# Performance work log

Hardware: AMD Instinct MI355X
Metric: run time of the kernel (lower is better)

The kernel has to match this reference:

```python
import jax, jax.numpy as jnp
import numpy as np

B, S, D, H = 4, 2048, 1024, 16
DH = D // H
NEG = -100000.0


def setup_inputs() -> dict:
    key = jax.random.key(0)
    ks = jax.random.split(key, 13)
    s = 1.0 / np.sqrt(D)
    inp = {
        'q': jax.random.normal(ks[0], (B, S, D), jnp.float32),
        'k': jax.random.normal(ks[1], (B, S, D), jnp.float32),
        'v': jax.random.normal(ks[2], (B, S, D), jnp.float32),
        'mask': jax.random.randint(ks[3], (B, 1, S, S), 0, 2).astype(bool),
        'wq_w': jax.random.normal(ks[4], (D, D), jnp.float32) * s,
        'wq_b': jnp.zeros((D,), jnp.float32),
        'wk_w': jax.random.normal(ks[5], (D, D), jnp.float32) * s,
        'wk_b': jnp.zeros((D,), jnp.float32),
        'wv_w': jax.random.normal(ks[6], (D, D), jnp.float32) * s,
        'wv_b': jnp.zeros((D,), jnp.float32),
        'wo_w': jax.random.normal(ks[7], (D, D), jnp.float32) * s,
        'wo_b': jnp.zeros((D,), jnp.float32),
    }
    return inp


def reference(q, k, v, mask, wq_w, wq_b, wk_w, wk_b, wv_w, wv_b, wo_w, wo_b):
    # torch Linear: y = x @ W^T + b
    qh = (q @ wq_w.T + wq_b).reshape(B, S, H, DH).transpose(0, 2, 1, 3)  # [B,H,S,DH]
    kh = (k @ wk_w.T + wk_b).reshape(B, S, H, DH).transpose(0, 2, 1, 3)
    vh = (v @ wv_w.T + wv_b).reshape(B, S, H, DH).transpose(0, 2, 1, 3)
    # NOTE: original code has NO 1/sqrt(d) scaling
    alpha = jnp.einsum('bhqd,bhkd->bhqk', qh, kh)  # [B,H,S,S]
    alpha = jnp.where(mask, NEG, alpha)
    score = jax.nn.softmax(alpha, axis=-1)
    x = jnp.einsum('bhqk,bhkd->bhqd', score, vh)
    x = x.transpose(0, 2, 1, 3).reshape(B, S, D)
    return x @ wo_w.T + wo_b
```

## Files before the change

### kernel.cpp

```cpp
#include <hip/hip_runtime.h>
#include <hip/hip_bf16.h>

#define B_ 4
#define S_ 2048
#define D_ 1024
#define H_ 16
#define NEGV (-100000.0f)
#define L2E 1.4426950408889634f

typedef __attribute__((ext_vector_type(8))) short short8;
typedef __attribute__((ext_vector_type(4))) float f32x4;
typedef unsigned short us;
typedef unsigned long long u64;

__device__ __forceinline__ us f2h(float f) {
  union { _Float16 h; us u; } c;
  c.h = (_Float16)f;
  return c.u;
}
__device__ __forceinline__ float exp2a(float x) {
  float r;
  asm("v_exp_f32 %0, %1" : "=v"(r) : "v"(x));
  return r;
}

__global__ void detect_mask_kernel(const int* __restrict__ mi, int* __restrict__ flag) {
  int t = threadIdx.x;
  bool bad = false;
  for (int i = t; i < 16384; i += 64) {
    int v = mi[i];
    bad = bad || (v != 0 && v != 1);
  }
  unsigned long long any = __ballot(bad);
  if (t == 0) flag[0] = (any != 0ull) ? 1 : 0;
}

__global__ __launch_bounds__(256) void pack_mask(const void* __restrict__ maskp,
                                                 const int* __restrict__ flag,
                                                 unsigned* __restrict__ pk) {
  int w = blockIdx.x * 256 + threadIdx.x;
  unsigned bits = 0;
  if (flag[0]) {
    const uint4* p = (const uint4*)((const unsigned char*)maskp + (size_t)w * 32);
#pragma unroll
    for (int q = 0; q < 2; ++q) {
      uint4 v = p[q];
      unsigned vv[4] = {v.x, v.y, v.z, v.w};
#pragma unroll
      for (int e = 0; e < 4; ++e) {
        unsigned byte4 = vv[e];
#pragma unroll
        for (int bb = 0; bb < 4; ++bb)
          bits |= (unsigned)(((byte4 >> (8 * bb)) & 0xffu) != 0) << (q * 16 + e * 4 + bb);
      }
    }
  } else {
    const uint4* p = (const uint4*)((const int*)maskp + (size_t)w * 32);
#pragma unroll
    for (int q = 0; q < 8; ++q) {
      uint4 v = p[q];
      bits |= (unsigned)(v.x != 0) << (q * 4 + 0);
      bits |= (unsigned)(v.y != 0) << (q * 4 + 1);
      bits |= (unsigned)(v.z != 0) << (q * 4 + 2);
      bits |= (unsigned)(v.w != 0) << (q * 4 + 3);
    }
  }
  pk[w] = bits;
}

__global__ __launch_bounds__(256) void cvt_f16x3(const float* __restrict__ i0,
                                                 const float* __restrict__ i1,
                                                 const float* __restrict__ i2,
                                                 us* __restrict__ o0, us* __restrict__ o1,
                                                 us* __restrict__ o2) {
  int z = blockIdx.x >> 12;
  int i = (blockIdx.x & 4095) * 256 + threadIdx.x;
  const float* in = z == 0 ? i0 : z == 1 ? i1 : i2;
  us* out = z == 0 ? o0 : z == 1 ? o1 : o2;
  float4 a = ((const float4*)in)[2 * i];
  float4 b = ((const float4*)in)[2 * i + 1];
  us u[8] = {f2h(a.x), f2h(a.y), f2h(a.z), f2h(a.w),
             f2h(b.x), f2h(b.y), f2h(b.z), f2h(b.w)};
  ((uint4*)out)[i] = *(uint4*)u;
}

__global__ __launch_bounds__(256) void cvt_w4(const float* __restrict__ w0,
                                              const float* __restrict__ w1,
                                              const float* __restrict__ w2,
                                              const float* __restrict__ w3,
                                              us* __restrict__ d0, us* __restrict__ d1,
                                              us* __restrict__ d2, us* __restrict__ d3) {
  int which = blockIdx.x >> 9;
  int i = (blockIdx.x & 511) * 256 + threadIdx.x;
  const float* w = which == 0 ? w0 : which == 1 ? w1 : which == 2 ? w2 : w3;
  us* d = which == 0 ? d0 : which == 1 ? d1 : which == 2 ? d2 : d3;
  float4 a = ((const float4*)w)[2 * i];
  float4 b = ((const float4*)w)[2 * i + 1];
  us u[8] = {f2h(a.x), f2h(a.y), f2h(a.z), f2h(a.w),
             f2h(b.x), f2h(b.y), f2h(b.z), f2h(b.w)};
  ((uint4*)d)[i] = *(uint4*)u;
}

__device__ __forceinline__ void gload16(const us* g, us* l) {
  __builtin_amdgcn_global_load_lds((const __attribute__((address_space(1))) void*)g,
                                   (__attribute__((address_space(3))) void*)l, 16, 0, 0);
}

__device__ __forceinline__ int swzb(int row, int c16) {
  return row * 128 + ((c16 ^ (row & 7)) << 4);
}

template <int OMODE>
__global__ __launch_bounds__(256) void gemm_mfma(
    const us* __restrict__ A0, const us* __restrict__ A1, const us* __restrict__ A2,
    const us* __restrict__ Wp0, const us* __restrict__ Wp1, const us* __restrict__ Wp2,
    const float* __restrict__ b0, const float* __restrict__ b1, const float* __restrict__ b2,
    void* __restrict__ C0, void* __restrict__ C1, void* __restrict__ C2,
    int M, int N, int K) {
  __shared__ __align__(16) us As[2][128 * 64];
  __shared__ __align__(16) us Ws[2][128 * 64];

  const int z = blockIdx.z;
  const us* A = z == 0 ? A0 : z == 1 ? A1 : A2;
  const us* W = z == 0 ? Wp0 : z == 1 ? Wp1 : Wp2;
  const float* bias = z == 0 ? b0 : z == 1 ? b1 : b2;
  void* Cp = z == 0 ? C0 : z == 1 ? C1 : C2;

  const int m0 = blockIdx.x * 128;
  const int n0 = blockIdx.y * 128;
  const int t = threadIdx.x;
  const int w = t >> 6, l = t & 63;
  const int l15 = l & 15, l4 = l >> 4;
  const int wm = w >> 1, wn = w & 1;

  int goff[4];
#pragma unroll
  for (int j = 0; j < 4; ++j) {
    int u = t + j * 256;
    int r = u >> 3, c8 = u & 7;
    int g = c8 ^ (r & 7);
    goff[j] = r * K + g * 8;
  }
  const us* Ag = A + (size_t)m0 * K;
  const us* Wg = W + (size_t)n0 * K;

  f32x4 acc[4][4];
#pragma unroll
  for (int m = 0; m < 4; ++m)
#pragma unroll
    for (int n = 0; n < 4; ++n) acc[m][n] = (f32x4){0.f, 0.f, 0.f, 0.f};

  auto stage = [&](int k0, int bb) {
#pragma unroll
    for (int j = 0; j < 4; ++j) {
      int u = t + j * 256;
      gload16(Ag + goff[j] + k0, &As[bb][u * 8]);
      gload16(Wg + goff[j] + k0, &Ws[bb][u * 8]);
    }
  };

  stage(0, 0);
  __syncthreads();
  int cur = 0;
  for (int k0 = 0; k0 < K; k0 += 64) {
    if (k0 + 64 < K) stage(k0 + 64, cur ^ 1);
#pragma unroll
    for (int ks = 0; ks < 2; ++ks) {
      short8 ah[4], bh_[4];
#pragma unroll
      for (int m = 0; m < 4; ++m)
        ah[m] = *(const short8*)((const char*)As[cur] + swzb(wm * 64 + m * 16 + l15, ks * 4 + l4));
#pragma unroll
      for (int n = 0; n < 4; ++n)
        bh_[n] = *(const short8*)((const char*)Ws[cur] + swzb(wn * 64 + n * 16 + l15, ks * 4 + l4));
#pragma unroll
      for (int m = 0; m < 4; ++m)
#pragma unroll
        for (int n = 0; n < 4; ++n)
          acc[m][n] = __builtin_amdgcn_mfma_f32_16x16x32_f16(ah[m], bh_[n], acc[m][n], 0, 0, 0);
    }
    __syncthreads();
    cur ^= 1;
  }

  float bv[4];
#pragma unroll
  for (int n = 0; n < 4; ++n) bv[n] = bias[n0 + wn * 64 + n * 16 + l15];

#pragma unroll
  for (int m = 0; m < 4; ++m) {
#pragma unroll
    for (int i = 0; i < 4; ++i) {
      int gm = m0 + wm * 64 + m * 16 + l4 * 4 + i;
#pragma unroll
      for (int n = 0; n < 4; ++n) {
        int gn = n0 + wn * 64 + n * 16 + l15;
        float o = acc[m][n][i] + bv[n];
        if constexpr (OMODE == 0) {
          ((float*)Cp)[(size_t)gm * N + gn] = o;
        } else {
          int b = gm >> 11, s = gm & (S_ - 1);
          int hh = gn >> 6, d = gn & 63;
          size_t idx = (((size_t)(b * H_ + hh) << 11) + s) * 64 + d;
          ((us*)Cp)[idx] = f2h(o);
        }
      }
    }
  }
}

__global__ __launch_bounds__(256) void transpose_v(const us* __restrict__ vh,
                                                   us* __restrict__ vt) {
  __shared__ us Ts[64][72];
  int blk = blockIdx.x;
  int bh = blk >> 5, s0 = (blk & 31) << 6;
  int t = threadIdx.x;
#pragma unroll
  for (int p = 0; p < 2; ++p) {
    int c = t + p * 256;
    int rs = c >> 3, c8 = c & 7;
    *(uint4*)&Ts[rs][c8 * 8] = *(const uint4*)(vh + ((size_t)bh * S_ + s0 + rs) * 64 + c8 * 8);
  }
  __syncthreads();
#pragma unroll
  for (int p = 0; p < 2; ++p) {
    int c = t + p * 256;
    int rd = c >> 3, s8 = c & 7;
    union { us u[8]; uint4 v; } tmp;
#pragma unroll
    for (int e = 0; e < 8; ++e) tmp.u[e] = Ts[s8 * 8 + e][rd];
    *(uint4*)(vt + ((size_t)bh * 64 + rd) * S_ + s0 + s8 * 8) = tmp.v;
  }
}

__device__ __forceinline__ int swz(int row, int bc) {
  return (row << 7) + (bc ^ ((row & 7) << 4));
}

__global__ __launch_bounds__(512) void attn_mfma(
    const us* __restrict__ qh, const us* __restrict__ kh,
    const us* __restrict__ vt, const unsigned* __restrict__ pk,
    us* __restrict__ xout) {
  __shared__ __align__(16) us Ks[2][4096];
  __shared__ __align__(16) us Vs[2][4096];
  __shared__ __align__(16) char Ps[16384];

  const int blk = ((blockIdx.x & 7) << 7) + (blockIdx.x >> 3);
  const int bh = blk >> 4;
  const int q0 = (blk & 15) << 7;
  const int b = bh >> 4, h = bh & (H_ - 1);
  const int t = threadIdx.x;
  const int w = t >> 6, l = t & 63;
  const int l15 = l & 15, l4 = l >> 4;

  short8 qf[2];
  {
    const size_t qbase = ((size_t)bh * S_ + q0 + 16 * w + l15) * 64 + l4 * 8;
    qf[0] = *(const short8*)(qh + qbase);
    qf[1] = *(const short8*)(qh + qbase + 32);
  }

  f32x4 accO[4];
#pragma unroll
  for (int jd = 0; jd < 4; ++jd) accO[jd] = (f32x4){0.f, 0.f, 0.f, 0.f};
  float m_i = -1e30f, l_p = 0.f;

  const int r_st = t >> 3, c_st = (t & 7) ^ ((t >> 3) & 7);
  const us* kh_src = kh + ((size_t)bh * S_ + r_st) * 64 + c_st * 8;
  const us* vt_src = vt + ((size_t)bh * 64 + r_st) * S_ + c_st * 8;

  auto stage = [&](int k0, int bb) {
    gload16(kh_src + (size_t)k0 * 64, &Ks[bb][t * 8]);
    gload16(vt_src + k0, &Vs[bb][t * 8]);
  };

  stage(0, 0);
  __syncthreads();
  int cur = 0;

  char* Pw = Ps + w * 2048;
  const int prowb = l15 * 128;
  const int rr7 = l15 & 7;
  const int bhalf = l4 >> 1;
  const int wsub = (l4 & 1) * 8;
  const unsigned* pb = pk + ((size_t)b * S_ + q0 + 16 * w + l15) * (S_ / 32);

  for (int k0 = 0; k0 < S_; k0 += 64) {
    uint2 mw = *(const uint2*)(pb + (k0 >> 5));
    if (k0 + 64 < S_) stage(k0 + 64, cur ^ 1);

    const char* KT = (const char*)Ks[cur];
    const char* VT = (const char*)Vs[cur];

    __builtin_amdgcn_s_setprio(1);
    f32x4 sj[4];
#pragma unroll
    for (int j = 0; j < 4; ++j) {
      f32x4 s = {0.f, 0.f, 0.f, 0.f};
#pragma unroll
      for (int c = 0; c < 2; ++c) {
        short8 kf = *(const short8*)(KT + swz(l15 + 16 * j, l4 * 16 + 64 * c));
        s = __builtin_amdgcn_mfma_f32_16x16x32_f16(kf, qf[c], s, 0, 0, 0);
      }
      sj[j] = s;
    }
    __builtin_amdgcn_s_setprio(0);

    float tm = -3e38f;
#pragma unroll
    for (int j = 0; j < 4; ++j) {
      unsigned wrd = (j < 2) ? mw.x : mw.y;
      int bb = ((j & 1) << 4) + (l4 << 2);
#pragma unroll
      for (int i = 0; i < 4; ++i) {
        float bf = (float)((wrd >> (bb + i)) & 1u);
        sj[j][i] = fmaf(bf, NEGV, sj[j][i]);
      }
      tm = fmaxf(tm, fmaxf(fmaxf(sj[j][0], sj[j][1]), fmaxf(sj[j][2], sj[j][3])));
    }
    tm = fmaxf(tm, __shfl_xor(tm, 16));
    tm = fmaxf(tm, __shfl_xor(tm, 32));

    if (__any(tm - m_i > 8.0f)) {
      float mnew = fmaxf(m_i, tm);
      float scl = exp2a((m_i - mnew) * L2E);
      l_p *= scl;
      m_i = mnew;
      float sr0 = __shfl(scl, 4 * l4 + 0);
      float sr1 = __shfl(scl, 4 * l4 + 1);
      float sr2 = __shfl(scl, 4 * l4 + 2);
      float sr3 = __shfl(scl, 4 * l4 + 3);
#pragma unroll
      for (int jd = 0; jd < 4; ++jd) {
        accO[jd][0] *= sr0; accO[jd][1] *= sr1;
        accO[jd][2] *= sr2; accO[jd][3] *= sr3;
      }
    }

    float ml2 = m_i * L2E;
#pragma unroll
    for (int j = 0; j < 4; ++j) {
      float p0 = exp2a(fmaf(sj[j][0], L2E, -ml2));
      float p1 = exp2a(fmaf(sj[j][1], L2E, -ml2));
      float p2 = exp2a(fmaf(sj[j][2], L2E, -ml2));
      float p3 = exp2a(fmaf(sj[j][3], L2E, -ml2));
      l_p += (p0 + p1) + (p2 + p3);
      unsigned d0, d1;
      asm("v_cvt_pkrtz_f16_f32 %0, %1, %2" : "=v"(d0) : "v"(p0), "v"(p1));
      asm("v_cvt_pkrtz_f16_f32 %0, %1, %2" : "=v"(d1) : "v"(p2), "v"(p3));
      int chunk = ((j << 1) | bhalf) ^ rr7;
      *(u64*)(Pw + prowb + (chunk << 4) + wsub) = (u64)d0 | ((u64)d1 << 32);
    }
    asm volatile("s_waitcnt lgkmcnt(0)" ::: "memory");
    __builtin_amdgcn_sched_barrier(0);

    __builtin_amdgcn_s_setprio(1);
#pragma unroll
    for (int kc = 0; kc < 2; ++kc) {
      int chR = (4 * kc + l4) ^ rr7;
      short8 pa = *(const short8*)(Pw + prowb + (chR << 4));
#pragma unroll
      for (int jd = 0; jd < 4; ++jd) {
        short8 vb = *(const short8*)(VT + swz(l15 + 16 * jd, l4 * 16 + 64 * kc));
        accO[jd] = __builtin_amdgcn_mfma_f32_16x16x32_f16(pa, vb, accO[jd], 0, 0, 0);
      }
    }
    __builtin_amdgcn_s_setprio(0);
    __syncthreads();
    cur ^= 1;
  }

  float lr = l_p;
  lr += __shfl_xor(lr, 16);
  lr += __shfl_xor(lr, 32);
  float inv0 = 1.f / __shfl(lr, 4 * l4 + 0);
  float inv1 = 1.f / __shfl(lr, 4 * l4 + 1);
  float inv2 = 1.f / __shfl(lr, 4 * l4 + 2);
  float inv3 = 1.f / __shfl(lr, 4 * l4 + 3);
  float invs[4] = {inv0, inv1, inv2, inv3};
#pragma unroll
  for (int i = 0; i < 4; ++i) {
    int row = q0 + 16 * w + l4 * 4 + i;
    size_t obase = ((size_t)b * S_ + row) * D_ + h * 64 + l15;
#pragma unroll
    for (int jd = 0; jd < 4; ++jd) xout[obase + 16 * jd] = f2h(accO[jd][i] * invs[i]);
  }
}

extern "C" void kernel_launch(void* const* d_in, const int* in_sizes, int n_in,
                              void* d_out, int out_size, void* d_ws, size_t ws_size,
                              hipStream_t stream) {
  const float* q = (const float*)d_in[0];
  const float* k = (const float*)d_in[1];
  const float* v = (const float*)d_in[2];
  const void* mask = d_in[3];
  const float* wq_w = (const float*)d_in[4];
  const float* wq_b = (const float*)d_in[5];
  const float* wk_w = (const float*)d_in[6];
  const float* wk_b = (const float*)d_in[7];
  const float* wv_w = (const float*)d_in[8];
  const float* wv_b = (const float*)d_in[9];
  const float* wo_w = (const float*)d_in[10];
  const float* wo_b = (const float*)d_in[11];

  const size_t NE = (size_t)B_ * S_ * D_;
  const size_t NW = (size_t)D_ * D_;
  const size_t PKB = (size_t)(B_ * S_ * (S_ / 32)) * 4;
  char* ws = (char*)d_ws;
  int* flag = (int*)ws;
  unsigned* pkb = (unsigned*)(ws + 256);
  us* base = (us*)(ws + 256 + PKB);

  detect_mask_kernel<<<1, 64, 0, stream>>>((const int*)mask, flag);
  pack_mask<<<2048, 256, 0, stream>>>(mask, flag, pkb);

  dim3 g2(64, 8, 2);
  dim3 g3(64, 8, 3);
  dim3 g1(64, 8, 1);

  const size_t fused_need = 256 + PKB + 6 * NE * 2 + 4 * NW * 2;
  if (ws_size >= fused_need) {
    us* A0 = base;
    us* A1 = A0 + NE;
    us* A2 = A1 + NE;
    us* A3 = A2 + NE;
    us* A4 = A3 + NE;
    us* A5 = A4 + NE;
    us* W0 = A5 + NE;
    us* W1 = W0 + NW;
    us* W2 = W1 + NW;
    us* W3 = W2 + NW;
    cvt_w4<<<2048, 256, 0, stream>>>(wq_w, wk_w, wv_w, wo_w, W0, W1, W2, W3);
    cvt_f16x3<<<3 * 4096, 256, 0, stream>>>(q, k, v, A0, A1, A2);
    gemm_mfma<2><<<g3, 256, 0, stream>>>(A0, A1, A2, W0, W1, W2, wq_b, wk_b, wv_b,
                                         A3, A4, A5, B_ * S_, D_, D_);
    transpose_v<<<2048, 256, 0, stream>>>(A5, A0);
    attn_mfma<<<1024, 512, 0, stream>>>(A3, A4, A0, pkb, A1);
    gemm_mfma<0><<<g1, 256, 0, stream>>>(A1, A1, A1, W3, W3, W3, wo_b, wo_b, wo_b,
                                         d_out, d_out, d_out, B_ * S_, D_, D_);
  } else {
    us* A0 = base;
    us* A1 = A0 + NE;
    us* A2 = A1 + NE;
    us* A3 = A2 + NE;
    us* A4 = A3 + NE;
    us* W0 = A4 + NE;
    us* W1 = W0 + NW;
    us* W2 = W1 + NW;
    us* W3 = W2 + NW;
    cvt_w4<<<2048, 256, 0, stream>>>(wq_w, wk_w, wv_w, wo_w, W0, W1, W2, W3);
    cvt_f16x3<<<2 * 4096, 256, 0, stream>>>(q, k, nullptr, A0, A1, nullptr);
    gemm_mfma<2><<<g2, 256, 0, stream>>>(A0, A1, nullptr, W0, W1, nullptr, wq_b, wk_b, nullptr,
                                         A2, A3, nullptr, B_ * S_, D_, D_);
    cvt_f16x3<<<4096, 256, 0, stream>>>(v, nullptr, nullptr, A0, nullptr, nullptr);
    gemm_mfma<2><<<g1, 256, 0, stream>>>(A0, nullptr, nullptr, W2, nullptr, nullptr,
                                         wv_b, nullptr, nullptr, A1, nullptr, nullptr,
                                         B_ * S_, D_, D_);
    transpose_v<<<2048, 256, 0, stream>>>(A1, A4);
    attn_mfma<<<1024, 512, 0, stream>>>(A2, A3, A4, pkb, A0);
    gemm_mfma<0><<<g1, 256, 0, stream>>>(A0, nullptr, nullptr, W3, nullptr, nullptr,
                                         wo_b, nullptr, nullptr, d_out, nullptr, nullptr,
                                         B_ * S_, D_, D_);
  }
}
```

Measured before the change: 364.1 us.

## Fuse V transpose into projection GEMM epilogue and streamline softmax masking

The V-projection GEMM now writes its output directly in transposed [bh, d, s] layout through a shared-memory staging tile, removing the separate transpose_v kernel launch and its extra global round trip. The attention kernel replaces the per-element bit-extract-and-fma masking with a 16-entry LDS lookup table added as a vector, and flattens the row-max reduction. Row-sum accumulation of the softmax probabilities moves to packed fp16 adds, which lowers per-iteration ALU work but loses some precision in the l sum.

```diff
diff --git a/kernel.cpp b/kernel.cpp
--- a/kernel.cpp
+++ b/kernel.cpp
@@ -10,6 +10,7 @@
 
 typedef __attribute__((ext_vector_type(8))) short short8;
 typedef __attribute__((ext_vector_type(4))) float f32x4;
+typedef _Float16 hf2 __attribute__((ext_vector_type(2)));
 typedef unsigned short us;
 typedef unsigned long long u64;
 
@@ -116,9 +117,8 @@
     const us* __restrict__ Wp0, const us* __restrict__ Wp1, const us* __restrict__ Wp2,
     const float* __restrict__ b0, const float* __restrict__ b1, const float* __restrict__ b2,
     void* __restrict__ C0, void* __restrict__ C1, void* __restrict__ C2,
-    int M, int N, int K) {
-  __shared__ __align__(16) us As[2][128 * 64];
-  __shared__ __align__(16) us Ws[2][128 * 64];
+    int M, int N, int K, int trans_z) {
+  __shared__ __align__(16) us SM[32768];
 
   const int z = blockIdx.z;
   const us* A = z == 0 ? A0 : z == 1 ? A1 : A2;
@@ -154,8 +154,8 @@
 #pragma unroll
     for (int j = 0; j < 4; ++j) {
       int u = t + j * 256;
-      gload16(Ag + goff[j] + k0, &As[bb][u * 8]);
-      gload16(Wg + goff[j] + k0, &Ws[bb][u * 8]);
+      gload16(Ag + goff[j] + k0, SM + bb * 8192 + u * 8);
+      gload16(Wg + goff[j] + k0, SM + 16384 + bb * 8192 + u * 8);
     }
   };
 
@@ -169,10 +169,12 @@
       short8 ah[4], bh_[4];
 #pragma unroll
       for (int m = 0; m < 4; ++m)
-        ah[m] = *(const short8*)((const char*)As[cur] + swzb(wm * 64 + m * 16 + l15, ks * 4 + l4));
+        ah[m] = *(const short8*)((const char*)(SM + cur * 8192) +
+                                 swzb(wm * 64 + m * 16 + l15, ks * 4 + l4));
 #pragma unroll
       for (int n = 0; n < 4; ++n)
-        bh_[n] = *(const short8*)((const char*)Ws[cur] + swzb(wn * 64 + n * 16 + l15, ks * 4 + l4));
+        bh_[n] = *(const short8*)((const char*)(SM + 16384 + cur * 8192) +
+                                  swzb(wn * 64 + n * 16 + l15, ks * 4 + l4));
 #pragma unroll
       for (int m = 0; m < 4; ++m)
 #pragma unroll
@@ -186,6 +188,33 @@
   float bv[4];
 #pragma unroll
   for (int n = 0; n < 4; ++n) bv[n] = bias[n0 + wn * 64 + n * 16 + l15];
+
+  if (OMODE == 2 && z == trans_z) {
+    us* T = SM;
+#pragma unroll
+    for (int n = 0; n < 4; ++n) {
+      int col = wn * 64 + n * 16 + l15;
+#pragma unroll
+      for (int m = 0; m < 4; ++m) {
+        int sr = wm * 64 + m * 16 + l4 * 4;
+#pragma unroll
+        for (int ip = 0; ip < 2; ++ip) {
+          us h0 = f2h(acc[m][n][2 * ip] + bv[n]);
+          us h1 = f2h(acc[m][n][2 * ip + 1] + bv[n]);
+          *(unsigned*)&T[col * 136 + sr + 2 * ip] = (unsigned)h0 | ((unsigned)h1 << 16);
+        }
+      }
+    }
+    __syncthreads();
+    const int b = m0 >> 11, sb = m0 & (S_ - 1);
+    const int colr = t >> 1, sc = (t & 1) << 6;
+    const int hh = (n0 >> 6) + (colr >> 6), d = colr & 63;
+    us* dst = (us*)Cp + (((size_t)(b * H_ + hh) << 6) + (size_t)d) * S_ + sb + sc;
+#pragma unroll
+    for (int p = 0; p < 8; ++p)
+      *(uint4*)(dst + p * 8) = *(const uint4*)&T[colr * 136 + sc + p * 8];
+    return;
+  }
 
 #pragma unroll
   for (int m = 0; m < 4; ++m) {
@@ -209,30 +238,6 @@
   }
 }
 
-__global__ __launch_bounds__(256) void transpose_v(const us* __restrict__ vh,
-                                                   us* __restrict__ vt) {
-  __shared__ us Ts[64][72];
-  int blk = blockIdx.x;
-  int bh = blk >> 5, s0 = (blk & 31) << 6;
-  int t = threadIdx.x;
-#pragma unroll
-  for (int p = 0; p < 2; ++p) {
-    int c = t + p * 256;
-    int rs = c >> 3, c8 = c & 7;
-    *(uint4*)&Ts[rs][c8 * 8] = *(const uint4*)(vh + ((size_t)bh * S_ + s0 + rs) * 64 + c8 * 8);
-  }
-  __syncthreads();
-#pragma unroll
-  for (int p = 0; p < 2; ++p) {
-    int c = t + p * 256;
-    int rd = c >> 3, s8 = c & 7;
-    union { us u[8]; uint4 v; } tmp;
-#pragma unroll
-    for (int e = 0; e < 8; ++e) tmp.u[e] = Ts[s8 * 8 + e][rd];
-    *(uint4*)(vt + ((size_t)bh * 64 + rd) * S_ + s0 + s8 * 8) = tmp.v;
-  }
-}
-
 __device__ __forceinline__ int swz(int row, int bc) {
   return (row << 7) + (bc ^ ((row & 7) << 4));
 }
@@ -244,6 +249,7 @@
   __shared__ __align__(16) us Ks[2][4096];
   __shared__ __align__(16) us Vs[2][4096];
   __shared__ __align__(16) char Ps[16384];
+  __shared__ __align__(16) float MLutF[64];
 
   const int blk = ((blockIdx.x & 7) << 7) + (blockIdx.x >> 3);
   const int bh = blk >> 4;
@@ -274,6 +280,7 @@
     gload16(vt_src + k0, &Vs[bb][t * 8]);
   };
 
+  if (t < 64) MLutF[t] = (((t >> 2) >> (t & 3)) & 1) ? NEGV : 0.f;
   stage(0, 0);
   __syncthreads();
   int cur = 0;
@@ -306,18 +313,20 @@
     }
     __builtin_amdgcn_s_setprio(0);
 
-    float tm = -3e38f;
 #pragma unroll
     for (int j = 0; j < 4; ++j) {
       unsigned wrd = (j < 2) ? mw.x : mw.y;
-      int bb = ((j & 1) << 4) + (l4 << 2);
-#pragma unroll
-      for (int i = 0; i < 4; ++i) {
-        float bf = (float)((wrd >> (bb + i)) & 1u);
-        sj[j][i] = fmaf(bf, NEGV, sj[j][i]);
-      }
-      tm = fmaxf(tm, fmaxf(fmaxf(sj[j][0], sj[j][1]), fmaxf(sj[j][2], sj[j][3])));
-    }
+      unsigned nib = (wrd >> (((j & 1) << 4) + (l4 << 2))) & 0xFu;
+      f32x4 lv = *(const f32x4*)&MLutF[nib << 2];
+      sj[j] = sj[j] + lv;
+    }
+
+    float c0 = fmaxf(fmaxf(sj[0][0], sj[0][1]), sj[0][2]);
+    float c1 = fmaxf(fmaxf(sj[0][3], sj[1][0]), sj[1][1]);
+    float c2 = fmaxf(fmaxf(sj[1][2], sj[1][3]), sj[2][0]);
+    float c3 = fmaxf(fmaxf(sj[2][1], sj[2][2]), sj[2][3]);
+    float c4 = fmaxf(fmaxf(sj[3][0], sj[3][1]), sj[3][2]);
+    float tm = fmaxf(fmaxf(fmaxf(c0, c1), c2), fmaxf(fmaxf(c3, c4), sj[3][3]));
     tm = fmaxf(tm, __shfl_xor(tm, 16));
     tm = fmaxf(tm, __shfl_xor(tm, 32));
 
@@ -338,19 +347,26 @@
     }
 
     float ml2 = m_i * L2E;
+    hf2 acc2;
+    acc2.x = (_Float16)0.f;
+    acc2.y = (_Float16)0.f;
 #pragma unroll
     for (int j = 0; j < 4; ++j) {
       float p0 = exp2a(fmaf(sj[j][0], L2E, -ml2));
       float p1 = exp2a(fmaf(sj[j][1], L2E, -ml2));
       float p2 = exp2a(fmaf(sj[j][2], L2E, -ml2));
       float p3 = exp2a(fmaf(sj[j][3], L2E, -ml2));
-      l_p += (p0 + p1) + (p2 + p3);
       unsigned d0, d1;
       asm("v_cvt_pkrtz_f16_f32 %0, %1, %2" : "=v"(d0) : "v"(p0), "v"(p1));
       asm("v_cvt_pkrtz_f16_f32 %0, %1, %2" : "=v"(d1) : "v"(p2), "v"(p3));
+      union { unsigned u; hf2 h; } c0u, c1u;
+      c0u.u = d0;
+      c1u.u = d1;
+      acc2 = acc2 + c0u.h + c1u.h;
       int chunk = ((j << 1) | bhalf) ^ rr7;
       *(u64*)(Pw + prowb + (chunk << 4) + wsub) = (u64)d0 | ((u64)d1 << 32);
     }
+    l_p += (float)acc2.x + (float)acc2.y;
     asm volatile("s_waitcnt lgkmcnt(0)" ::: "memory");
     __builtin_amdgcn_sched_barrier(0);
 
@@ -433,11 +449,10 @@
     cvt_w4<<<2048, 256, 0, stream>>>(wq_w, wk_w, wv_w, wo_w, W0, W1, W2, W3);
     cvt_f16x3<<<3 * 4096, 256, 0, stream>>>(q, k, v, A0, A1, A2);
     gemm_mfma<2><<<g3, 256, 0, stream>>>(A0, A1, A2, W0, W1, W2, wq_b, wk_b, wv_b,
-                                         A3, A4, A5, B_ * S_, D_, D_);
-    transpose_v<<<2048, 256, 0, stream>>>(A5, A0);
-    attn_mfma<<<1024, 512, 0, stream>>>(A3, A4, A0, pkb, A1);
-    gemm_mfma<0><<<g1, 256, 0, stream>>>(A1, A1, A1, W3, W3, W3, wo_b, wo_b, wo_b,
-                                         d_out, d_out, d_out, B_ * S_, D_, D_);
+                                         A3, A4, A5, B_ * S_, D_, D_, 2);
+    attn_mfma<<<1024, 512, 0, stream>>>(A3, A4, A5, pkb, A0);
+    gemm_mfma<0><<<g1, 256, 0, stream>>>(A0, A0, A0, W3, W3, W3, wo_b, wo_b, wo_b,
+                                         d_out, d_out, d_out, B_ * S_, D_, D_, -1);
   } else {
     us* A0 = base;
     us* A1 = A0 + NE;
@@ -451,15 +466,14 @@
     cvt_w4<<<2048, 256, 0, stream>>>(wq_w, wk_w, wv_w, wo_w, W0, W1, W2, W3);
     cvt_f16x3<<<2 * 4096, 256, 0, stream>>>(q, k, nullptr, A0, A1, nullptr);
     gemm_mfma<2><<<g2, 256, 0, stream>>>(A0, A1, nullptr, W0, W1, nullptr, wq_b, wk_b, nullptr,
-                                         A2, A3, nullptr, B_ * S_, D_, D_);
+                                         A2, A3, nullptr, B_ * S_, D_, D_, -1);
     cvt_f16x3<<<4096, 256, 0, stream>>>(v, nullptr, nullptr, A0, nullptr, nullptr);
     gemm_mfma<2><<<g1, 256, 0, stream>>>(A0, nullptr, nullptr, W2, nullptr, nullptr,
-                                         wv_b, nullptr, nullptr, A1, nullptr, nullptr,
-                                         B_ * S_, D_, D_);
-    transpose_v<<<2048, 256, 0, stream>>>(A1, A4);
+                                         wv_b, nullptr, nullptr, A4, nullptr, nullptr,
+                                         B_ * S_, D_, D_, 0);
     attn_mfma<<<1024, 512, 0, stream>>>(A2, A3, A4, pkb, A0);
     gemm_mfma<0><<<g1, 256, 0, stream>>>(A0, nullptr, nullptr, W3, nullptr, nullptr,
                                          wo_b, nullptr, nullptr, d_out, nullptr, nullptr,
-                                         B_ * S_, D_, D_);
-  }
-}
+                                         B_ * S_, D_, D_, -1);
+  }
+}
```

Result: faster. 346.6 us (-4.8%).
